# Kernel tuning notes

Hardware: AMD Instinct MI355X
Metric: run time of the kernel (lower is better)

## Reference

```python
import jax, jax.numpy as jnp
import numpy as np

N = 16384
H = 2048
E = 8
I_PER_E = 8192 // E  # expert_intermediate_size = 1024


def setup_inputs() -> dict:
    key = jax.random.key(0)
    k1, k2, k3, k4 = jax.random.split(key, 4)
    hidden_states = jax.random.normal(k1, (N, H), dtype=jnp.float32)
    # sort_idx is a permutation of [0, N): tokens sorted by expert assignment
    sort_idx = jax.random.permutation(k2, N).astype(jnp.int64)
    # kaiming_uniform_ with a=sqrt(5): bound = sqrt(6/((1+a^2)*fan_in)) = 1/sqrt(fan_in)
    bound = 1.0 / np.sqrt(H)
    gate_up_proj = jax.random.uniform(k3, (E, H, 2 * I_PER_E), dtype=jnp.float32,
                                      minval=-bound, maxval=bound)
    # original inits down_proj to zeros; use small random so backward is non-trivial
    down_proj = jax.random.normal(k4, (E, I_PER_E, H), dtype=jnp.float32) * 0.02
    return {"hidden_states": hidden_states, "sort_idx": sort_idx,
            "gate_up_proj": gate_up_proj, "down_proj": down_proj}


def reference(hidden_states, sort_idx, gate_up_proj, down_proj):
    n, h = hidden_states.shape
    e = gate_up_proj.shape[0]
    chunk = n // e
    # gather tokens into expert order: [E, chunk, H]
    sorted_x = hidden_states[sort_idx].reshape(e, chunk, h)
    # fused gate+up grouped GEMM: [E, chunk, 2*I/E]
    gu = jnp.einsum('ech,ehf->ecf', sorted_x, gate_up_proj)
    gate, up = jnp.split(gu, 2, axis=-1)
    activated = jax.nn.silu(gate) * up  # [E, chunk, I/E]
    sorted_out = jnp.einsum('eci,eih->ech', activated, down_proj).reshape(n, h)
    # scatter back: out[sort_idx] = sorted_out
    out = jnp.zeros((n, h), dtype=sorted_out.dtype).at[sort_idx].set(sorted_out)
    return out
```

## Files before the change

### kernel.cpp

```cpp
#include <hip/hip_runtime.h>
#include <hip/hip_bf16.h>

#define N_TOK 16384
#define H_DIM 2048
#define NE 8
#define CHUNK 2048
#define IPE 1024
#define F2 2048

typedef __bf16 bf16;
typedef bf16 bf16x8 __attribute__((ext_vector_type(8)));
typedef float f32x4 __attribute__((ext_vector_type(4)));

typedef __attribute__((address_space(1))) void gvoid;
typedef __attribute__((address_space(3))) void svoid;

__device__ __forceinline__ void gload_lds16(const void* g, void* l) {
  __builtin_amdgcn_global_load_lds((gvoid*)g, (svoid*)l, 16, 0, 0);
}
__device__ __forceinline__ f32x4 MF(bf16x8 a, bf16x8 b, f32x4 c) {
  return __builtin_amdgcn_mfma_f32_16x16x32_bf16(a, b, c, 0, 0, 0);
}

#define BAR() __builtin_amdgcn_s_barrier()
#define LGKM0() asm volatile("s_waitcnt lgkmcnt(0)" ::: "memory")
#define VM6() asm volatile("s_waitcnt vmcnt(6)" ::: "memory")
#define VM0() asm volatile("s_waitcnt vmcnt(0)" ::: "memory")
#define PRIO(x) __builtin_amdgcn_s_setprio(x)

__global__ __launch_bounds__(256) void k_gather(
    const float* __restrict__ x, const int* __restrict__ sidx,
    bf16* __restrict__ xs) {
  int row = blockIdx.x;
  int src = sidx[row];
  const float4* ip = (const float4*)(x + (size_t)src * H_DIM);
  int t = threadIdx.x;
  float4 f0 = ip[t * 2], f1 = ip[t * 2 + 1];
  bf16x8 v;
  v[0] = (bf16)f0.x; v[1] = (bf16)f0.y; v[2] = (bf16)f0.z; v[3] = (bf16)f0.w;
  v[4] = (bf16)f1.x; v[5] = (bf16)f1.y; v[6] = (bf16)f1.z; v[7] = (bf16)f1.w;
  *(bf16x8*)(xs + (size_t)row * H_DIM + t * 8) = v;
}

__global__ __launch_bounds__(256) void k_tr_w1(const float* __restrict__ in,
                                               bf16* __restrict__ out) {
  int e = blockIdx.z;
  int fB = blockIdx.x;
  int hB = blockIdx.y;
  __shared__ bf16 lds[64][68];
  int tx = threadIdx.x & 63;
  int ty = threadIdx.x >> 6;
  const float* ip = in + ((size_t)e * H_DIM + hB * 64) * F2;
  int scol = (tx < 32) ? (fB * 32 + tx) : (1024 + fB * 32 + (tx - 32));
#pragma unroll
  for (int p = 0; p < 16; ++p) {
    int hl = p * 4 + ty;
    lds[hl][tx] = (bf16)ip[(size_t)hl * F2 + scol];
  }
  __syncthreads();
  bf16* op = out + ((size_t)e * F2 + fB * 64) * H_DIM + hB * 64;
#pragma unroll
  for (int p = 0; p < 16; ++p) {
    int fl = p * 4 + ty;
    int g = fl >> 4, w = fl & 15;
    int lcol = ((g >> 1) << 4) + w + ((g & 1) << 5);
    op[(size_t)fl * H_DIM + tx] = lds[tx][lcol];
  }
}

__global__ __launch_bounds__(256) void k_tr_w2(const float* __restrict__ in,
                                               bf16* __restrict__ out) {
  int e = blockIdx.z;
  int hB = blockIdx.x;
  int iB = blockIdx.y;
  __shared__ bf16 lds[64][68];
  int tx = threadIdx.x & 63;
  int ty = threadIdx.x >> 6;
  const float* ip = in + (size_t)e * IPE * H_DIM + (size_t)iB * 64 * H_DIM + hB * 64;
#pragma unroll
  for (int p = 0; p < 16; ++p) {
    int il = p * 4 + ty;
    lds[il][tx] = (bf16)ip[(size_t)il * H_DIM + tx];
  }
  __syncthreads();
  bf16* op = out + (size_t)e * H_DIM * IPE + (size_t)hB * 64 * IPE + iB * 64;
#pragma unroll
  for (int p = 0; p < 16; ++p) {
    int hl = p * 4 + ty;
    op[(size_t)hl * IPE + tx] = lds[tx][hl];
  }
}

template <int KDIM, bool SILU>
__global__ __launch_bounds__(512, 2) void k_gemm8(
    const bf16* __restrict__ Aptr, const bf16* __restrict__ Bptr,
    const int* __restrict__ sidx, bf16* __restrict__ act,
    float* __restrict__ fout) {
  extern __shared__ char smem[];
  const int tid = threadIdx.x, lane = tid & 63, wv = tid >> 6;
  const int wm = wv >> 2, wn = wv & 3;
  constexpr int NT = KDIM / 64;

  int swzwg = (blockIdx.x & 7) * (gridDim.x >> 3) + (blockIdx.x >> 3);
  const int e = swzwg >> 6, bm = (swzwg >> 3) & 7, bn = swzwg & 7;

  const char* Ab = (const char*)(Aptr + ((size_t)e * CHUNK + bm * 256) * KDIM);
  const char* Bb = (const char*)(Bptr + ((size_t)e * 2048 + bn * 256) * KDIM);

  const int L0 = wv * 1024 + lane * 16;
  const int lin0 = L0 ^ (((L0 >> 7) & 7) << 4);
  const int srow0 = lin0 >> 7, scolb = lin0 & 127;

  const int rA = lane & 15;
  const int swzr = (rA & 7) << 4;
  const int cb = (lane >> 4) * 16;

  f32x4 acc[8][4] = {};

  auto stage = [&](int buf, int mat, int half, int kt) {
    const char* gb = (mat == 0) ? Ab : Bb;
    char* ld = smem + buf * 65536 + mat * 32768 + half * 16384 + wv * 1024;
    size_t rb = (size_t)(half * 128 + srow0) * (KDIM * 2) + (size_t)kt * 128 + scolb;
    gload_lds16(gb + rb, ld);
    gload_lds16(gb + rb + (size_t)64 * (KDIM * 2), ld + 8192);
  };
  auto ldA = [&](int buf, int mi, int ks) {
    int lin = ((mi * 16 + rA) << 7) + ks * 64 + cb;
    return *(const bf16x8*)(smem + buf * 65536 + wm * 16384 + (lin ^ swzr));
  };
  auto ldB = [&](int buf, int ni, int ks) {
    int lin = (((wn & 1) * 64 + ni * 16 + rA) << 7) + ks * 64 + cb;
    return *(const bf16x8*)(smem + buf * 65536 + 32768 + (wn >> 1) * 16384 + (lin ^ swzr));
  };

  stage(0, 1, 0, 0); stage(0, 1, 1, 0); stage(0, 0, 0, 0); stage(0, 0, 1, 0);
  stage(1, 1, 0, 1); stage(1, 1, 1, 1); stage(1, 0, 0, 1);
  VM6();
  BAR();

  for (int t = 0; t < NT; ++t) {
    const int cur = t & 1, nxt = cur ^ 1;
    bf16x8 b0[4], b1[4], a0[4], a1[4], a2[4];
#pragma unroll
    for (int ni = 0; ni < 4; ++ni) b0[ni] = ldB(cur, ni, 0);
#pragma unroll
    for (int mi = 0; mi < 4; ++mi) a0[mi] = ldA(cur, mi, 0);
#pragma unroll
    for (int ni = 0; ni < 4; ++ni) b1[ni] = ldB(cur, ni, 1);
    if (t + 1 < NT) stage(nxt, 0, 1, t + 1);
    BAR();
    PRIO(1);
#pragma unroll
    for (int mi = 0; mi < 4; ++mi)
#pragma unroll
      for (int ni = 0; ni < 4; ++ni) acc[mi][ni] = MF(a0[mi], b0[ni], acc[mi][ni]);
    PRIO(0);
    LGKM0();
    BAR();
#pragma unroll
    for (int mi = 0; mi < 4; ++mi) a1[mi] = ldA(cur, mi, 1);
#pragma unroll
    for (int mi = 0; mi < 4; ++mi) a2[mi] = ldA(cur, 4 + mi, 0);
    if (t + 2 < NT) stage(cur, 1, 0, t + 2);
    BAR();
    PRIO(1);
#pragma unroll
    for (int mi = 0; mi < 4; ++mi)
#pragma unroll
      for (int ni = 0; ni < 4; ++ni) acc[mi][ni] = MF(a1[mi], b1[ni], acc[mi][ni]);
    PRIO(0);
    LGKM0();
    BAR();
#pragma unroll
    for (int mi = 0; mi < 4; ++mi) a0[mi] = ldA(cur, 4 + mi, 1);
    if (t + 2 < NT) stage(cur, 1, 1, t + 2);
    BAR();
    PRIO(1);
#pragma unroll
    for (int mi = 0; mi < 4; ++mi)
#pragma unroll
      for (int ni = 0; ni < 4; ++ni) acc[4 + mi][ni] = MF(a2[mi], b0[ni], acc[4 + mi][ni]);
    PRIO(0);
    LGKM0();
    BAR();
    if (t + 2 < NT) {
      stage(cur, 0, 0, t + 2);
      VM6();
    } else if (t + 1 < NT) {
      VM0();
    }
    BAR();
    PRIO(1);
#pragma unroll
    for (int mi = 0; mi < 4; ++mi)
#pragma unroll
      for (int ni = 0; ni < 4; ++ni) acc[4 + mi][ni] = MF(a0[mi], b1[ni], acc[4 + mi][ni]);
    PRIO(0);
    BAR();
  }

  if constexpr (SILU) {
    bf16* actp = act + ((size_t)e * CHUNK + bm * 256 + wm * 128) * IPE;
    const int r0 = (lane >> 4) * 4;
    const int c0 = bn * 128 + wn * 32 + (lane & 15);
#pragma unroll
    for (int mi = 0; mi < 8; ++mi)
#pragma unroll
      for (int p = 0; p < 2; ++p) {
        f32x4 g = acc[mi][2 * p], u = acc[mi][2 * p + 1];
#pragma unroll
        for (int r = 0; r < 4; ++r) {
          float gv = g[r];
          float a = gv / (1.f + __expf(-gv)) * u[r];
          actp[(size_t)(mi * 16 + r0 + r) * IPE + c0 + p * 16] = (bf16)a;
        }
      }
  } else {
    const int* sp = sidx + e * CHUNK + bm * 256 + wm * 128;
    const int r0 = (lane >> 4) * 4;
    const int c0 = bn * 256 + wn * 64 + (lane & 15);
#pragma unroll
    for (int mi = 0; mi < 8; ++mi)
#pragma unroll
      for (int r = 0; r < 4; ++r) {
        int dst = sp[mi * 16 + r0 + r];
        float* op = fout + (size_t)dst * H_DIM + c0;
#pragma unroll
        for (int ni = 0; ni < 4; ++ni) op[ni * 16] = acc[mi][ni][r];
      }
  }
}

extern "C" void kernel_launch(void* const* d_in, const int* in_sizes, int n_in,
                              void* d_out, int out_size, void* d_ws, size_t ws_size,
                              hipStream_t stream) {
  const float* hidden = (const float*)d_in[0];
  const int* sidx = (const int*)d_in[1];
  const float* w1 = (const float*)d_in[2];
  const float* w2 = (const float*)d_in[3];
  float* out = (float*)d_out;

  char* ws = (char*)d_ws;
  bf16* xs  = (bf16*)(ws);
  bf16* w1t = (bf16*)(ws + (size_t)67108864);
  bf16* act = (bf16*)(ws + (size_t)134217728);
  bf16* w2t = (bf16*)(ws);

  hipFuncSetAttribute((const void*)k_gemm8<H_DIM, true>,
                      hipFuncAttributeMaxDynamicSharedMemorySize, 131072);
  hipFuncSetAttribute((const void*)k_gemm8<IPE, false>,
                      hipFuncAttributeMaxDynamicSharedMemorySize, 131072);

  k_gather<<<dim3(N_TOK), 256, 0, stream>>>(hidden, sidx, xs);
  k_tr_w1<<<dim3(32, 32, NE), 256, 0, stream>>>(w1, w1t);
  k_gemm8<H_DIM, true><<<dim3(512), 512, 131072, stream>>>(xs, w1t, nullptr, act, nullptr);
  k_tr_w2<<<dim3(32, 16, NE), 256, 0, stream>>>(w2, w2t);
  k_gemm8<IPE, false><<<dim3(512), 512, 131072, stream>>>(act, w2t, sidx, nullptr, out);
}
```

Measured before the change: 308.2 us.

## Fuse token gather into first GEMM and merge weight transposes

Drops the separate gather/convert kernel. The first GEMM now reads fp32 hidden rows through sort_idx, converts them to bf16 in registers and writes them to LDS. Both weight transposes merge into one launch with vectorized 16-byte stores. The GEMM moves from a 256x256 tile with a K-step of 64 and about 128KB of LDS to a 256x128 (first GEMM: 256x64 output) tile with a K-step of 32, 48KB of static LDS and a simple double-buffered loop. That gives four blocks per CU and twice as many blocks in the grid. The cost is more barriers per unit of work, less register reuse per MFMA, and fp32 A loads going through registers instead of direct global-to-LDS loads.

```diff
diff --git a/kernel.cpp b/kernel.cpp
--- a/kernel.cpp
+++ b/kernel.cpp
@@ -21,212 +21,203 @@
 __device__ __forceinline__ f32x4 MF(bf16x8 a, bf16x8 b, f32x4 c) {
   return __builtin_amdgcn_mfma_f32_16x16x32_bf16(a, b, c, 0, 0, 0);
 }
-
-#define BAR() __builtin_amdgcn_s_barrier()
-#define LGKM0() asm volatile("s_waitcnt lgkmcnt(0)" ::: "memory")
-#define VM6() asm volatile("s_waitcnt vmcnt(6)" ::: "memory")
-#define VM0() asm volatile("s_waitcnt vmcnt(0)" ::: "memory")
-#define PRIO(x) __builtin_amdgcn_s_setprio(x)
-
-__global__ __launch_bounds__(256) void k_gather(
-    const float* __restrict__ x, const int* __restrict__ sidx,
-    bf16* __restrict__ xs) {
-  int row = blockIdx.x;
-  int src = sidx[row];
-  const float4* ip = (const float4*)(x + (size_t)src * H_DIM);
-  int t = threadIdx.x;
-  float4 f0 = ip[t * 2], f1 = ip[t * 2 + 1];
-  bf16x8 v;
-  v[0] = (bf16)f0.x; v[1] = (bf16)f0.y; v[2] = (bf16)f0.z; v[3] = (bf16)f0.w;
-  v[4] = (bf16)f1.x; v[5] = (bf16)f1.y; v[6] = (bf16)f1.z; v[7] = (bf16)f1.w;
-  *(bf16x8*)(xs + (size_t)row * H_DIM + t * 8) = v;
-}
-
-__global__ __launch_bounds__(256) void k_tr_w1(const float* __restrict__ in,
-                                               bf16* __restrict__ out) {
-  int e = blockIdx.z;
-  int fB = blockIdx.x;
-  int hB = blockIdx.y;
+__device__ __forceinline__ int swz(int x) { return x ^ (((x >> 7) & 7) << 4); }
+
+__global__ __launch_bounds__(256) void k_prep(const float* __restrict__ w1,
+                                              const float* __restrict__ w2,
+                                              bf16* __restrict__ w1t,
+                                              bf16* __restrict__ w2t) {
   __shared__ bf16 lds[64][68];
-  int tx = threadIdx.x & 63;
-  int ty = threadIdx.x >> 6;
-  const float* ip = in + ((size_t)e * H_DIM + hB * 64) * F2;
-  int scol = (tx < 32) ? (fB * 32 + tx) : (1024 + fB * 32 + (tx - 32));
-#pragma unroll
-  for (int p = 0; p < 16; ++p) {
-    int hl = p * 4 + ty;
-    lds[hl][tx] = (bf16)ip[(size_t)hl * F2 + scol];
-  }
-  __syncthreads();
-  bf16* op = out + ((size_t)e * F2 + fB * 64) * H_DIM + hB * 64;
-#pragma unroll
-  for (int p = 0; p < 16; ++p) {
-    int fl = p * 4 + ty;
+  int b = blockIdx.x;
+  int tx = threadIdx.x & 63, ty = threadIdx.x >> 6;
+  if (b < 8192) {
+    int fB = b & 31, hB = (b >> 5) & 31, e = b >> 10;
+    const float* ip = w1 + ((size_t)e * H_DIM + hB * 64) * F2;
+    int scol = (tx < 32) ? (fB * 32 + tx) : (1024 + fB * 32 + (tx - 32));
+#pragma unroll
+    for (int p = 0; p < 16; ++p) {
+      int hl = p * 4 + ty;
+      lds[hl][tx] = (bf16)ip[(size_t)hl * F2 + scol];
+    }
+    __syncthreads();
+    int fl = threadIdx.x >> 2, hseg = (threadIdx.x & 3) * 16;
     int g = fl >> 4, w = fl & 15;
     int lcol = ((g >> 1) << 4) + w + ((g & 1) << 5);
-    op[(size_t)fl * H_DIM + tx] = lds[tx][lcol];
-  }
-}
-
-__global__ __launch_bounds__(256) void k_tr_w2(const float* __restrict__ in,
-                                               bf16* __restrict__ out) {
-  int e = blockIdx.z;
-  int hB = blockIdx.x;
-  int iB = blockIdx.y;
-  __shared__ bf16 lds[64][68];
-  int tx = threadIdx.x & 63;
-  int ty = threadIdx.x >> 6;
-  const float* ip = in + (size_t)e * IPE * H_DIM + (size_t)iB * 64 * H_DIM + hB * 64;
-#pragma unroll
-  for (int p = 0; p < 16; ++p) {
-    int il = p * 4 + ty;
-    lds[il][tx] = (bf16)ip[(size_t)il * H_DIM + tx];
-  }
-  __syncthreads();
-  bf16* op = out + (size_t)e * H_DIM * IPE + (size_t)hB * 64 * IPE + iB * 64;
-#pragma unroll
-  for (int p = 0; p < 16; ++p) {
-    int hl = p * 4 + ty;
-    op[(size_t)hl * IPE + tx] = lds[tx][hl];
-  }
-}
-
-template <int KDIM, bool SILU>
-__global__ __launch_bounds__(512, 2) void k_gemm8(
-    const bf16* __restrict__ Aptr, const bf16* __restrict__ Bptr,
+    bf16 v[16];
+#pragma unroll
+    for (int j = 0; j < 16; ++j) v[j] = lds[hseg + j][lcol];
+    bf16* op = w1t + ((size_t)e * F2 + fB * 64 + fl) * H_DIM + hB * 64 + hseg;
+    *(bf16x8*)op = *(bf16x8*)&v[0];
+    *(bf16x8*)(op + 8) = *(bf16x8*)&v[8];
+  } else {
+    int i2 = b - 8192;
+    int hB = i2 & 31, iB = (i2 >> 5) & 15, e = i2 >> 9;
+    const float* ip = w2 + (size_t)e * IPE * H_DIM + (size_t)iB * 64 * H_DIM + hB * 64;
+#pragma unroll
+    for (int p = 0; p < 16; ++p) {
+      int il = p * 4 + ty;
+      lds[il][tx] = (bf16)ip[(size_t)il * H_DIM + tx];
+    }
+    __syncthreads();
+    int hl = threadIdx.x >> 2, iseg = (threadIdx.x & 3) * 16;
+    bf16 v[16];
+#pragma unroll
+    for (int j = 0; j < 16; ++j) v[j] = lds[iseg + j][hl];
+    bf16* op = w2t + ((size_t)e * H_DIM + hB * 64 + hl) * IPE + iB * 64 + iseg;
+    *(bf16x8*)op = *(bf16x8*)&v[0];
+    *(bf16x8*)(op + 8) = *(bf16x8*)&v[8];
+  }
+}
+
+template <int KDIM, bool FUSED_A, bool SILU>
+__global__ __launch_bounds__(512, 4) void k_gemm(
+    const void* __restrict__ Asrc, const bf16* __restrict__ Bptr,
     const int* __restrict__ sidx, bf16* __restrict__ act,
     float* __restrict__ fout) {
-  extern __shared__ char smem[];
+  __shared__ char smem[49152];
   const int tid = threadIdx.x, lane = tid & 63, wv = tid >> 6;
   const int wm = wv >> 2, wn = wv & 3;
-  constexpr int NT = KDIM / 64;
-
-  int swzwg = (blockIdx.x & 7) * (gridDim.x >> 3) + (blockIdx.x >> 3);
-  const int e = swzwg >> 6, bm = (swzwg >> 3) & 7, bn = swzwg & 7;
-
-  const char* Ab = (const char*)(Aptr + ((size_t)e * CHUNK + bm * 256) * KDIM);
-  const char* Bb = (const char*)(Bptr + ((size_t)e * 2048 + bn * 256) * KDIM);
-
-  const int L0 = wv * 1024 + lane * 16;
-  const int lin0 = L0 ^ (((L0 >> 7) & 7) << 4);
-  const int srow0 = lin0 >> 7, scolb = lin0 & 127;
+  constexpr int NT = KDIM / 32;
+
+  const int bid = blockIdx.x;
+  const int swg = (bid & 7) * 128 + (bid >> 3);
+  const int e = swg >> 7, bm = (swg >> 4) & 7, bn = swg & 15;
+
+  const int PB = tid * 16;
+  const int LB = swz(PB);
+  const char* Bsrc = (const char*)Bptr +
+      ((size_t)e * 2048 + bn * 128 + (LB >> 6)) * (KDIM * 2) + (LB & 63);
+
+  const int aR = tid >> 1, akh = tid & 1;
+  const float* Afp = nullptr;
+  int AwP0 = 0, AwP1 = 0;
+  const char* Ag0 = nullptr;
+  const char* Ag1 = nullptr;
+  int AgP0 = 0, AgP1 = 0;
+  if constexpr (FUSED_A) {
+    int tok = sidx[e * CHUNK + bm * 256 + aR];
+    Afp = (const float*)Asrc + (size_t)tok * H_DIM + akh * 16;
+    int L0 = (aR >> 1) * 128 + (aR & 1) * 64 + akh * 32;
+    AwP0 = swz(L0);
+    AwP1 = swz(L0 + 16);
+  } else {
+    AgP0 = wv * 2048 + lane * 16;
+    AgP1 = AgP0 + 1024;
+    int L0 = swz(AgP0), L1 = swz(AgP1);
+    Ag0 = (const char*)Asrc +
+        ((size_t)e * CHUNK + bm * 256 + (L0 >> 6)) * (KDIM * 2) + (L0 & 63);
+    Ag1 = (const char*)Asrc +
+        ((size_t)e * CHUNK + bm * 256 + (L1 >> 6)) * (KDIM * 2) + (L1 & 63);
+  }
 
   const int rA = lane & 15;
-  const int swzr = (rA & 7) << 4;
   const int cb = (lane >> 4) * 16;
 
-  f32x4 acc[8][4] = {};
-
-  auto stage = [&](int buf, int mat, int half, int kt) {
-    const char* gb = (mat == 0) ? Ab : Bb;
-    char* ld = smem + buf * 65536 + mat * 32768 + half * 16384 + wv * 1024;
-    size_t rb = (size_t)(half * 128 + srow0) * (KDIM * 2) + (size_t)kt * 128 + scolb;
-    gload_lds16(gb + rb, ld);
-    gload_lds16(gb + rb + (size_t)64 * (KDIM * 2), ld + 8192);
-  };
-  auto ldA = [&](int buf, int mi, int ks) {
-    int lin = ((mi * 16 + rA) << 7) + ks * 64 + cb;
-    return *(const bf16x8*)(smem + buf * 65536 + wm * 16384 + (lin ^ swzr));
-  };
-  auto ldB = [&](int buf, int ni, int ks) {
-    int lin = (((wn & 1) * 64 + ni * 16 + rA) << 7) + ks * 64 + cb;
-    return *(const bf16x8*)(smem + buf * 65536 + 32768 + (wn >> 1) * 16384 + (lin ^ swzr));
-  };
-
-  stage(0, 1, 0, 0); stage(0, 1, 1, 0); stage(0, 0, 0, 0); stage(0, 0, 1, 0);
-  stage(1, 1, 0, 1); stage(1, 1, 1, 1); stage(1, 0, 0, 1);
-  VM6();
-  BAR();
+  f32x4 acc[8][2] = {};
+  float4 al0, al1, al2, al3;
+
+  auto loadA = [&](int kt) {
+    const float* s = Afp + kt * 32;
+    al0 = *(const float4*)s;
+    al1 = *(const float4*)(s + 4);
+    al2 = *(const float4*)(s + 8);
+    al3 = *(const float4*)(s + 12);
+  };
+  auto writeA = [&](int buf) {
+    bf16x8 t0, t1;
+    t0[0] = (bf16)al0.x; t0[1] = (bf16)al0.y; t0[2] = (bf16)al0.z; t0[3] = (bf16)al0.w;
+    t0[4] = (bf16)al1.x; t0[5] = (bf16)al1.y; t0[6] = (bf16)al1.z; t0[7] = (bf16)al1.w;
+    t1[0] = (bf16)al2.x; t1[1] = (bf16)al2.y; t1[2] = (bf16)al2.z; t1[3] = (bf16)al2.w;
+    t1[4] = (bf16)al3.x; t1[5] = (bf16)al3.y; t1[6] = (bf16)al3.z; t1[7] = (bf16)al3.w;
+    *(bf16x8*)(smem + buf * 24576 + AwP0) = t0;
+    *(bf16x8*)(smem + buf * 24576 + AwP1) = t1;
+  };
+  auto stageA = [&](int buf, int kt) {
+    gload_lds16(Ag0 + kt * 64, smem + buf * 24576 + AgP0);
+    gload_lds16(Ag1 + kt * 64, smem + buf * 24576 + AgP1);
+  };
+  auto stageB = [&](int buf, int kt) {
+    gload_lds16(Bsrc + kt * 64, smem + buf * 24576 + 16384 + PB);
+  };
+  auto ldA = [&](int buf, int mi) {
+    int R = wm * 128 + mi * 16 + rA;
+    int L = (R >> 1) * 128 + (R & 1) * 64 + cb;
+    return *(const bf16x8*)(smem + buf * 24576 + swz(L));
+  };
+  auto ldB = [&](int buf, int ni) {
+    int f = wn * 32 + ni * 16 + rA;
+    int L = (f >> 1) * 128 + (f & 1) * 64 + cb;
+    return *(const bf16x8*)(smem + buf * 24576 + 16384 + swz(L));
+  };
+
+  if constexpr (FUSED_A) {
+    loadA(0);
+    stageB(0, 0);
+    writeA(0);
+  } else {
+    stageA(0, 0);
+    stageB(0, 0);
+  }
+  __syncthreads();
 
   for (int t = 0; t < NT; ++t) {
     const int cur = t & 1, nxt = cur ^ 1;
-    bf16x8 b0[4], b1[4], a0[4], a1[4], a2[4];
-#pragma unroll
-    for (int ni = 0; ni < 4; ++ni) b0[ni] = ldB(cur, ni, 0);
-#pragma unroll
-    for (int mi = 0; mi < 4; ++mi) a0[mi] = ldA(cur, mi, 0);
-#pragma unroll
-    for (int ni = 0; ni < 4; ++ni) b1[ni] = ldB(cur, ni, 1);
-    if (t + 1 < NT) stage(nxt, 0, 1, t + 1);
-    BAR();
-    PRIO(1);
-#pragma unroll
-    for (int mi = 0; mi < 4; ++mi)
-#pragma unroll
-      for (int ni = 0; ni < 4; ++ni) acc[mi][ni] = MF(a0[mi], b0[ni], acc[mi][ni]);
-    PRIO(0);
-    LGKM0();
-    BAR();
-#pragma unroll
-    for (int mi = 0; mi < 4; ++mi) a1[mi] = ldA(cur, mi, 1);
-#pragma unroll
-    for (int mi = 0; mi < 4; ++mi) a2[mi] = ldA(cur, 4 + mi, 0);
-    if (t + 2 < NT) stage(cur, 1, 0, t + 2);
-    BAR();
-    PRIO(1);
-#pragma unroll
-    for (int mi = 0; mi < 4; ++mi)
-#pragma unroll
-      for (int ni = 0; ni < 4; ++ni) acc[mi][ni] = MF(a1[mi], b1[ni], acc[mi][ni]);
-    PRIO(0);
-    LGKM0();
-    BAR();
-#pragma unroll
-    for (int mi = 0; mi < 4; ++mi) a0[mi] = ldA(cur, 4 + mi, 1);
-    if (t + 2 < NT) stage(cur, 1, 1, t + 2);
-    BAR();
-    PRIO(1);
-#pragma unroll
-    for (int mi = 0; mi < 4; ++mi)
-#pragma unroll
-      for (int ni = 0; ni < 4; ++ni) acc[4 + mi][ni] = MF(a2[mi], b0[ni], acc[4 + mi][ni]);
-    PRIO(0);
-    LGKM0();
-    BAR();
-    if (t + 2 < NT) {
-      stage(cur, 0, 0, t + 2);
-      VM6();
-    } else if (t + 1 < NT) {
-      VM0();
-    }
-    BAR();
-    PRIO(1);
-#pragma unroll
-    for (int mi = 0; mi < 4; ++mi)
-#pragma unroll
-      for (int ni = 0; ni < 4; ++ni) acc[4 + mi][ni] = MF(a0[mi], b1[ni], acc[4 + mi][ni]);
-    PRIO(0);
-    BAR();
+    if (t + 1 < NT) {
+      if constexpr (FUSED_A) {
+        loadA(t + 1);
+        stageB(nxt, t + 1);
+      } else {
+        stageA(nxt, t + 1);
+        stageB(nxt, t + 1);
+      }
+    }
+    bf16x8 B0 = ldB(cur, 0), B1 = ldB(cur, 1);
+    {
+      bf16x8 A0 = ldA(cur, 0), A1 = ldA(cur, 1), A2 = ldA(cur, 2), A3 = ldA(cur, 3);
+      acc[0][0] = MF(A0, B0, acc[0][0]); acc[0][1] = MF(A0, B1, acc[0][1]);
+      acc[1][0] = MF(A1, B0, acc[1][0]); acc[1][1] = MF(A1, B1, acc[1][1]);
+      acc[2][0] = MF(A2, B0, acc[2][0]); acc[2][1] = MF(A2, B1, acc[2][1]);
+      acc[3][0] = MF(A3, B0, acc[3][0]); acc[3][1] = MF(A3, B1, acc[3][1]);
+    }
+    {
+      bf16x8 A4 = ldA(cur, 4), A5 = ldA(cur, 5), A6 = ldA(cur, 6), A7 = ldA(cur, 7);
+      acc[4][0] = MF(A4, B0, acc[4][0]); acc[4][1] = MF(A4, B1, acc[4][1]);
+      acc[5][0] = MF(A5, B0, acc[5][0]); acc[5][1] = MF(A5, B1, acc[5][1]);
+      acc[6][0] = MF(A6, B0, acc[6][0]); acc[6][1] = MF(A6, B1, acc[6][1]);
+      acc[7][0] = MF(A7, B0, acc[7][0]); acc[7][1] = MF(A7, B1, acc[7][1]);
+    }
+    if constexpr (FUSED_A) {
+      if (t + 1 < NT) writeA(nxt);
+    }
+    __syncthreads();
   }
 
   if constexpr (SILU) {
     bf16* actp = act + ((size_t)e * CHUNK + bm * 256 + wm * 128) * IPE;
     const int r0 = (lane >> 4) * 4;
-    const int c0 = bn * 128 + wn * 32 + (lane & 15);
-#pragma unroll
-    for (int mi = 0; mi < 8; ++mi)
-#pragma unroll
-      for (int p = 0; p < 2; ++p) {
-        f32x4 g = acc[mi][2 * p], u = acc[mi][2 * p + 1];
-#pragma unroll
-        for (int r = 0; r < 4; ++r) {
-          float gv = g[r];
-          float a = gv / (1.f + __expf(-gv)) * u[r];
-          actp[(size_t)(mi * 16 + r0 + r) * IPE + c0 + p * 16] = (bf16)a;
-        }
+    const int c0 = bn * 64 + wn * 16 + rA;
+#pragma unroll
+    for (int mi = 0; mi < 8; ++mi) {
+      f32x4 g = acc[mi][0], u = acc[mi][1];
+#pragma unroll
+      for (int r = 0; r < 4; ++r) {
+        float gv = g[r];
+        float a = gv / (1.f + __expf(-gv)) * u[r];
+        actp[(size_t)(mi * 16 + r0 + r) * IPE + c0] = (bf16)a;
       }
+    }
   } else {
     const int* sp = sidx + e * CHUNK + bm * 256 + wm * 128;
     const int r0 = (lane >> 4) * 4;
-    const int c0 = bn * 256 + wn * 64 + (lane & 15);
+    const int c0 = bn * 128 + wn * 32 + rA;
 #pragma unroll
     for (int mi = 0; mi < 8; ++mi)
 #pragma unroll
       for (int r = 0; r < 4; ++r) {
         int dst = sp[mi * 16 + r0 + r];
         float* op = fout + (size_t)dst * H_DIM + c0;
-#pragma unroll
-        for (int ni = 0; ni < 4; ++ni) op[ni * 16] = acc[mi][ni][r];
+        op[0] = acc[mi][0][r];
+        op[16] = acc[mi][1][r];
       }
   }
 }
@@ -241,19 +232,13 @@
   float* out = (float*)d_out;
 
   char* ws = (char*)d_ws;
-  bf16* xs  = (bf16*)(ws);
-  bf16* w1t = (bf16*)(ws + (size_t)67108864);
-  bf16* act = (bf16*)(ws + (size_t)134217728);
-  bf16* w2t = (bf16*)(ws);
-
-  hipFuncSetAttribute((const void*)k_gemm8<H_DIM, true>,
-                      hipFuncAttributeMaxDynamicSharedMemorySize, 131072);
-  hipFuncSetAttribute((const void*)k_gemm8<IPE, false>,
-                      hipFuncAttributeMaxDynamicSharedMemorySize, 131072);
-
-  k_gather<<<dim3(N_TOK), 256, 0, stream>>>(hidden, sidx, xs);
-  k_tr_w1<<<dim3(32, 32, NE), 256, 0, stream>>>(w1, w1t);
-  k_gemm8<H_DIM, true><<<dim3(512), 512, 131072, stream>>>(xs, w1t, nullptr, act, nullptr);
-  k_tr_w2<<<dim3(32, 16, NE), 256, 0, stream>>>(w2, w2t);
-  k_gemm8<IPE, false><<<dim3(512), 512, 131072, stream>>>(act, w2t, sidx, nullptr, out);
-}
+  bf16* w1t = (bf16*)(ws);
+  bf16* w2t = (bf16*)(ws + (size_t)67108864);
+  bf16* act = (bf16*)(ws + (size_t)100663296);
+
+  k_prep<<<dim3(12288), 256, 0, stream>>>(w1, w2, w1t, w2t);
+  k_gemm<H_DIM, true, true><<<dim3(1024), 512, 0, stream>>>(
+      hidden, w1t, sidx, act, nullptr);
+  k_gemm<IPE, false, false><<<dim3(1024), 512, 0, stream>>>(
+      act, w2t, sidx, nullptr, out);
+}
```

Measured after the change: 380.2 us. 1.23x slower.
